# Kernel optimization log

Hardware: AMD Instinct MI355X
Metric: run time of the kernel (lower is better)

Reference implementation:

```python
import jax, jax.numpy as jnp
import numpy as np

B, S, D, H, HD, F = 2, 2048, 2048, 16, 128, 8192
EPS = 1e-5
THETA = 10000.0
NEG = -1e30


def _rmsnorm(x, w):
    v = jnp.mean(jnp.square(x.astype(jnp.float32)), axis=-1, keepdims=True)
    return (x.astype(jnp.float32) * jax.lax.rsqrt(v + EPS)).astype(x.dtype) * w


def _rope(x):
    # x: [B, S, H, HD]; llama-style rotate-half rotary embedding
    inv_freq = 1.0 / (THETA ** (jnp.arange(0, HD, 2, dtype=jnp.float32) / HD))
    ang = jnp.arange(S, dtype=jnp.float32)[:, None] * inv_freq[None, :]  # [S, HD//2]
    cos = jnp.concatenate([jnp.cos(ang), jnp.cos(ang)], axis=-1)[None, :, None, :]
    sin = jnp.concatenate([jnp.sin(ang), jnp.sin(ang)], axis=-1)[None, :, None, :]
    x1, x2 = jnp.split(x, 2, axis=-1)
    return x * cos + jnp.concatenate([-x2, x1], axis=-1) * sin


def _mlp(x, wg, wu, wd):
    # SiLU-gated HiggsAudioMLP: down(silu(gate(x)) * up(x))
    return (jax.nn.silu(x @ wg) * (x @ wu)) @ wd


def setup_inputs() -> dict:
    key = jax.random.key(0)
    ks = jax.random.split(key, 12)
    std = 0.02
    p = lambda k, shape: jax.random.normal(k, shape, dtype=jnp.float32) * std
    return {
        "hidden_states": jax.random.normal(ks[0], (B, S, D), dtype=jnp.float32),
        "audio_out_mask": jax.random.randint(ks[1], (B, S), 0, 2).astype(bool),
        "wq": p(ks[2], (D, H * HD)),
        "wk": p(ks[3], (D, H * HD)),
        "wv": p(ks[4], (D, H * HD)),
        "wo": p(ks[5], (H * HD, D)),
        "input_ln_w": jnp.ones((D,), jnp.float32),
        "post_ln_w": jnp.ones((D,), jnp.float32),
        "audio_post_ln_w": jnp.ones((D,), jnp.float32),
        "w_gate_t": p(ks[6], (D, F)),
        "w_up_t": p(ks[7], (D, F)),
        "w_down_t": p(ks[8], (F, D)),
        "w_gate_a": p(ks[9], (D, F)),
        "w_up_a": p(ks[10], (D, F)),
        "w_down_a": p(ks[11], (F, D)),
    }


def reference(hidden_states, audio_out_mask, wq, wk, wv, wo, input_ln_w, post_ln_w,
              audio_post_ln_w, w_gate_t, w_up_t, w_down_t, w_gate_a, w_up_a, w_down_a):
    # ---- self-attention block ----
    residual = hidden_states
    h = _rmsnorm(hidden_states, input_ln_w)
    q = _rope((h @ wq).reshape(B, S, H, HD))
    k = _rope((h @ wk).reshape(B, S, H, HD))
    v = (h @ wv).reshape(B, S, H, HD)
    scores = jnp.einsum("bqhd,bkhd->bhqk", q, k) / float(np.sqrt(HD))
    causal = jnp.tril(jnp.ones((S, S), bool))
    scores = jnp.where(causal[None, None], scores, NEG)
    attn = jax.nn.softmax(scores, axis=-1)
    ctx = jnp.einsum("bhqk,bkhd->bqhd", attn, v).reshape(B, S, H * HD)
    hidden_states = residual + ctx @ wo
    # ---- dual FFN, per-token routed by audio_out_mask ----
    residual = hidden_states
    text_out = _mlp(_rmsnorm(hidden_states, post_ln_w), w_gate_t, w_up_t, w_down_t)
    audio_out = _mlp(_rmsnorm(hidden_states, audio_post_ln_w), w_gate_a, w_up_a, w_down_a)
    return residual + jnp.where(audio_out_mask[..., None], audio_out, text_out)
```

## Files before the change

kernel.cpp:

```cpp
#include <hip/hip_runtime.h>


#define BB 2
#define SS 2048
#define DD 2048
#define HH 16
#define HDD 128
#define FF 8192
#define TT (BB*SS)
#define RPAD 4608

typedef unsigned short ushort_t;
typedef __bf16 bf16x8 __attribute__((ext_vector_type(8)));
typedef float f32x4 __attribute__((ext_vector_type(4)));

#define DEV static __device__ __forceinline__

DEV float bf2f(ushort_t u) { __bf16 b; __builtin_memcpy(&b, &u, 2); return (float)b; }
DEV ushort_t f2bf(float f) { __bf16 b = (__bf16)f; ushort_t u; __builtin_memcpy(&u, &b, 2); return u; }

DEV void gl_lds16(const ushort_t* g, ushort_t* l) {
    __builtin_amdgcn_global_load_lds((const __attribute__((address_space(1))) void*)g,
                                     (__attribute__((address_space(3))) void*)l, 16, 0, 0);
}

#define BARRIER() do { asm volatile("" ::: "memory"); __builtin_amdgcn_s_barrier(); asm volatile("" ::: "memory"); } while (0)
#define LGKM0()   asm volatile("s_waitcnt lgkmcnt(0)" ::: "memory")

__global__ __launch_bounds__(256) void partition_k(const unsigned char* __restrict__ raw,
                                                   int* __restrict__ perm,
                                                   int* __restrict__ header) {
    __shared__ int flag;
    __shared__ int ct[256], ca[256], st[256], sa[256];
    __shared__ int Nt_s, Na_s;
    const int tid = threadIdx.x;
    if (tid == 0) flag = 0;
    __syncthreads();
    int any = 0;
    for (int i = tid; i < TT; i += 256)
        if ((i & 3) != 0 && raw[i] != 0) any = 1;
    if (any) atomicOr(&flag, 1);
    __syncthreads();
    const int is_byte = flag;
    auto mget = [&](int r) -> int {
        return is_byte ? (raw[r] != 0) : (((const int*)raw)[r] != 0);
    };
    int c0 = 0, c1 = 0;
#pragma unroll
    for (int i = 0; i < 16; ++i) {
        if (mget(tid * 16 + i)) c1++; else c0++;
    }
    ct[tid] = c0; ca[tid] = c1;
    __syncthreads();
    if (tid == 0) {
        int at = 0, aa = 0;
        for (int i = 0; i < 256; ++i) {
            st[i] = at; at += ct[i];
            sa[i] = aa; aa += ca[i];
        }
        Nt_s = at; Na_s = aa;
    }
    __syncthreads();
    const int Nt = Nt_s, Na = Na_s;
    const int A0 = (Nt + 255) & ~255;
    const int live = A0 + ((Na + 255) & ~255);
    int pt = st[tid], pa = A0 + sa[tid];
#pragma unroll
    for (int i = 0; i < 16; ++i) {
        const int r = tid * 16 + i;
        if (mget(r)) perm[pa++] = r; else perm[pt++] = r;
    }
    for (int i = Nt + tid; i < A0; i += 256) perm[i] = -1;
    for (int i = A0 + Na + tid; i < RPAD; i += 256) perm[i] = -1;
    if (tid == 0) { header[0] = Nt; header[1] = A0; header[2] = Na; header[3] = live; }
}

struct ConvSeg { const float* in; ushort_t* out; int K, N, cumEnd; };
struct ConvArgs { ConvSeg s[10]; };

__global__ __launch_bounds__(256) void convw_all(ConvArgs a) {
    __shared__ float t[32][33];
    int bid = blockIdx.x;
    int i = 0;
    while (bid >= a.s[i].cumEnd) ++i;
    const int base = (i == 0) ? 0 : a.s[i - 1].cumEnd;
    const int local = bid - base;
    const float* __restrict__ in = a.s[i].in;
    ushort_t* __restrict__ out = a.s[i].out;
    const int K = a.s[i].K, N = a.s[i].N;
    const int ntile = N >> 5;
    const int n0 = (local % ntile) * 32, k0 = (local / ntile) * 32;
    const int tx = threadIdx.x & 31, ty = threadIdx.x >> 5;
#pragma unroll
    for (int j = 0; j < 4; ++j)
        t[ty + 8 * j][tx] = in[(size_t)(k0 + ty + 8 * j) * N + n0 + tx];
    __syncthreads();
#pragma unroll
    for (int j = 0; j < 4; ++j)
        out[(size_t)(n0 + ty + 8 * j) * K + k0 + tx] = f2bf(t[tx][ty + 8 * j]);
}

__global__ __launch_bounds__(256) void rmsnorm_k(const float* __restrict__ x,
                                                 const float* __restrict__ wt,
                                                 ushort_t* __restrict__ out) {
    const int row = blockIdx.x, tid = threadIdx.x;
    const float4* xr = (const float4*)(x + (size_t)row * DD);
    float4 v0 = xr[tid * 2], v1 = xr[tid * 2 + 1];
    float ss = v0.x * v0.x + v0.y * v0.y + v0.z * v0.z + v0.w * v0.w
             + v1.x * v1.x + v1.y * v1.y + v1.z * v1.z + v1.w * v1.w;
#pragma unroll
    for (int d = 1; d < 64; d <<= 1) ss += __shfl_xor(ss, d);
    __shared__ float red[4];
    if ((tid & 63) == 0) red[tid >> 6] = ss;
    __syncthreads();
    const float tot = red[0] + red[1] + red[2] + red[3];
    const float sc = rsqrtf(tot * (1.0f / DD) + 1e-5f);
    const float4* wr = (const float4*)wt;
    float4 w0 = wr[tid * 2], w1 = wr[tid * 2 + 1];
    ushort_t* o = out + (size_t)row * DD + tid * 8;
    o[0] = f2bf(v0.x * sc * w0.x); o[1] = f2bf(v0.y * sc * w0.y);
    o[2] = f2bf(v0.z * sc * w0.z); o[3] = f2bf(v0.w * sc * w0.w);
    o[4] = f2bf(v1.x * sc * w1.x); o[5] = f2bf(v1.y * sc * w1.y);
    o[6] = f2bf(v1.z * sc * w1.z); o[7] = f2bf(v1.w * sc * w1.w);
}

__global__ __launch_bounds__(256) void rmsnorm_gather(const float* __restrict__ x,
                                                      const float* __restrict__ wt_text,
                                                      const float* __restrict__ wt_audio,
                                                      const int* __restrict__ perm,
                                                      const int* __restrict__ header,
                                                      ushort_t* __restrict__ out) {
    const int i = blockIdx.x, tid = threadIdx.x;
    const int p = perm[i];
    ushort_t* o = out + (size_t)i * DD + tid * 8;
    if (p < 0) {
#pragma unroll
        for (int j = 0; j < 8; ++j) o[j] = 0;
        return;
    }
    const float* wt = (i < header[1]) ? wt_text : wt_audio;
    const float4* xr = (const float4*)(x + (size_t)p * DD);
    float4 v0 = xr[tid * 2], v1 = xr[tid * 2 + 1];
    float ss = v0.x * v0.x + v0.y * v0.y + v0.z * v0.z + v0.w * v0.w
             + v1.x * v1.x + v1.y * v1.y + v1.z * v1.z + v1.w * v1.w;
#pragma unroll
    for (int d = 1; d < 64; d <<= 1) ss += __shfl_xor(ss, d);
    __shared__ float red[4];
    if ((tid & 63) == 0) red[tid >> 6] = ss;
    __syncthreads();
    const float tot = red[0] + red[1] + red[2] + red[3];
    const float sc = rsqrtf(tot * (1.0f / DD) + 1e-5f);
    const float4* wr = (const float4*)wt;
    float4 w0 = wr[tid * 2], w1 = wr[tid * 2 + 1];
    o[0] = f2bf(v0.x * sc * w0.x); o[1] = f2bf(v0.y * sc * w0.y);
    o[2] = f2bf(v0.z * sc * w0.z); o[3] = f2bf(v0.w * sc * w0.w);
    o[4] = f2bf(v1.x * sc * w1.x); o[5] = f2bf(v1.y * sc * w1.y);
    o[6] = f2bf(v1.z * sc * w1.z); o[7] = f2bf(v1.w * sc * w1.w);
}

__global__ __launch_bounds__(256) void rope_tab(float* __restrict__ cosb,
                                                float* __restrict__ sinb) {
    const int idx = blockIdx.x * 256 + threadIdx.x;
    const int s = idx >> 6, i = idx & 63;
    const float inv = powf(10000.0f, -(float)i * (1.0f / 64.0f));
    const float ang = (float)s * inv;
    cosb[idx] = cosf(ang);
    sinb[idx] = sinf(ang);
}

__global__ __launch_bounds__(256) void rope_qk(ushort_t* __restrict__ qb,
                                               ushort_t* __restrict__ kb,
                                               const float* __restrict__ cosb,
                                               const float* __restrict__ sinb) {
    const int gid = blockIdx.x * 256 + threadIdx.x;
    ushort_t* x = (gid < TT * 1024) ? qb : kb;
    const int g = gid & (TT * 1024 - 1);
    const int row = g >> 10, p = g & 1023;
    const int h = p >> 6, d = p & 63;
    const int s = row & (SS - 1);
    const size_t base = (size_t)row * DD + h * HDD + d;
    const float x1 = bf2f(x[base]), x2 = bf2f(x[base + 64]);
    const float c = cosb[s * 64 + d], sn = sinb[s * 64 + d];
    x[base]      = f2bf(x1 * c - x2 * sn);
    x[base + 64] = f2bf(x2 * c + x1 * sn);
}

template <int EPI>
__global__ __launch_bounds__(512, 2) void gemm_nt8(
    const ushort_t* __restrict__ A, const ushort_t* __restrict__ W,
    int K, ushort_t* __restrict__ o0, ushort_t* __restrict__ o1,
    ushort_t* __restrict__ o2, float* __restrict__ Cf,
    const float* __restrict__ resid) {
    const int nwg = gridDim.x * gridDim.y;
    int bid = blockIdx.y * gridDim.x + blockIdx.x;
    bid = (bid & 7) * (nwg >> 3) + (bid >> 3);
    const int bxx = bid % gridDim.x;
    const int byy = bid / gridDim.x;
    const int m0 = byy * 256;
    int kind = 0, n0;
    const ushort_t* B;
    if (EPI == 0) {
        kind = bxx >> 4;
        n0 = (bxx & 15) * 128;
        B = W + (size_t)kind * DD * DD + (size_t)n0 * K;
    } else {
        n0 = bxx * 128;
        B = W + (size_t)n0 * K;
    }
    __shared__ ushort_t smem[49152];
    const int tid = threadIdx.x;
    const int w = tid >> 6, lane = tid & 63;
    const int wm = w >> 2, wn = w & 3;
    const int f16 = lane & 15, g4 = lane >> 4;
    const int rl = tid >> 3;
    const int cc8 = (((tid & 7) ^ ((tid >> 3) & 7)) * 8);
    const ushort_t* gA = A + (size_t)m0 * K;

    auto stageAq = [&](int buf, int k0, int q) {
        gl_lds16(gA + (size_t)(q * 64 + rl) * K + k0 + cc8,
                 &smem[buf * 24576 + q * 4096 + w * 512]);
    };
    auto stageB2 = [&](int buf, int k0) {
#pragma unroll
        for (int j = 0; j < 2; ++j)
            gl_lds16(B + (size_t)(j * 64 + rl) * K + k0 + cc8,
                     &smem[buf * 24576 + 16384 + j * 4096 + w * 512]);
    };

    const int aBase = (wm * 128 + f16) * 64;
    const int bBase = (wn * 32 + f16) * 64;
    int cswz[2];
    cswz[0] = ((g4 ^ (f16 & 7)) * 8);
    cswz[1] = (((4 + g4) ^ (f16 & 7)) * 8);

    f32x4 acc[8][2] = {};
    bf16x8 af[4][2], bfr[2][2];

    stageAq(0, 0, 0); stageAq(0, 0, 1); stageAq(0, 0, 2); stageAq(0, 0, 3);
    stageB2(0, 0);
    stageAq(1, 64, 0); stageAq(1, 64, 2); stageB2(1, 64);
    asm volatile("s_waitcnt vmcnt(4)" ::: "memory");
    BARRIER();

    const int nt = K / 64;
    for (int t = 0; t < nt; ++t) {
        const int cur = t & 1;
        const int ab = cur * 24576, bb = cur * 24576 + 16384;
#pragma unroll
        for (int m = 0; m < 4; ++m)
#pragma unroll
            for (int ks = 0; ks < 2; ++ks)
                af[m][ks] = *(const bf16x8*)&smem[ab + aBase + m * 1024 + cswz[ks]];
#pragma unroll
        for (int np = 0; np < 2; ++np)
#pragma unroll
            for (int ks = 0; ks < 2; ++ks)
                bfr[np][ks] = *(const bf16x8*)&smem[bb + bBase + np * 1024 + cswz[ks]];
        if (t + 1 < nt) {
            stageAq(1 - cur, (t + 1) * 64, 1);
            stageAq(1 - cur, (t + 1) * 64, 3);
        }
        BARRIER();
        LGKM0();
        __builtin_amdgcn_s_setprio(1);
#pragma unroll
        for (int m = 0; m < 4; ++m)
#pragma unroll
            for (int np = 0; np < 2; ++np)
#pragma unroll
                for (int ks = 0; ks < 2; ++ks)
                    acc[m][np] = __builtin_amdgcn_mfma_f32_16x16x32_bf16(af[m][ks], bfr[np][ks], acc[m][np], 0, 0, 0);
        __builtin_amdgcn_s_setprio(0);
        BARRIER();
#pragma unroll
        for (int m = 0; m < 4; ++m)
#pragma unroll
            for (int ks = 0; ks < 2; ++ks)
                af[m][ks] = *(const bf16x8*)&smem[ab + aBase + (4 + m) * 1024 + cswz[ks]];
        if (t + 2 < nt) {
            stageAq(cur, (t + 2) * 64, 0);
            stageAq(cur, (t + 2) * 64, 2);
            stageB2(cur, (t + 2) * 64);
        }
        BARRIER();
        LGKM0();
        __builtin_amdgcn_s_setprio(1);
#pragma unroll
        for (int m = 0; m < 4; ++m)
#pragma unroll
            for (int np = 0; np < 2; ++np)
#pragma unroll
                for (int ks = 0; ks < 2; ++ks)
                    acc[4 + m][np] = __builtin_amdgcn_mfma_f32_16x16x32_bf16(af[m][ks], bfr[np][ks], acc[4 + m][np], 0, 0, 0);
        __builtin_amdgcn_s_setprio(0);
        if (t + 2 < nt) { asm volatile("s_waitcnt vmcnt(4)" ::: "memory"); }
        else            { asm volatile("s_waitcnt vmcnt(0)" ::: "memory"); }
        BARRIER();
    }

#pragma unroll
    for (int m = 0; m < 8; ++m)
#pragma unroll
        for (int np = 0; np < 2; ++np)
#pragma unroll
            for (int j = 0; j < 4; ++j) {
                const int r = m0 + wm * 128 + m * 16 + g4 * 4 + j;
                const int c = n0 + wn * 32 + np * 16 + f16;
                const float v = acc[m][np][j];
                if (EPI == 0) {
                    const ushort_t vb = f2bf(v);
                    if (kind == 0)      o0[(size_t)r * DD + c] = vb;
                    else if (kind == 1) o1[(size_t)r * DD + c] = vb;
                    else {
                        const int b = r >> 11, s = r & (SS - 1), h = c >> 7, d = c & 127;
                        o2[(((size_t)(b * HH + h) * HDD + d) << 11) + s] = vb;
                    }
                } else {
                    const size_t idx = (size_t)r * DD + c;
                    Cf[idx] = resid[idx] + v;
                }
            }
}

__global__ __launch_bounds__(256, 2) void gemm_down_c(
    const ushort_t* __restrict__ A, const ushort_t* __restrict__ Bt_text,
    const ushort_t* __restrict__ Bt_audio, float* __restrict__ C,
    const int* __restrict__ perm, const int* __restrict__ header) {
    const int m0 = blockIdx.y * 128;
    if (m0 >= header[3]) return;
    const ushort_t* Bt = (m0 >= header[1]) ? Bt_audio : Bt_text;
    __shared__ ushort_t As[128 * 32];
    __shared__ ushort_t Bs[128 * 32];
    const int tid = threadIdx.x;
    const int w = tid >> 6, lane = tid & 63;
    const int n0 = blockIdx.x * 128;
    const int wr = w >> 1, wc = w & 1;
    f32x4 acc[4][4] = {};
    const ushort_t* gA = A + (size_t)m0 * FF;
    const ushort_t* gB = Bt + (size_t)n0 * FF;
    const int c0 = tid, c1 = 256 + tid;
    const int r0 = c0 >> 2, o0 = (c0 & 3) * 8;
    const int r1 = c1 >> 2, o1 = (c1 & 3) * 8;
    ushort_t* lA0 = &As[(w * 64) * 8];
    ushort_t* lA1 = &As[(256 + w * 64) * 8];
    ushort_t* lB0 = &Bs[(w * 64) * 8];
    ushort_t* lB1 = &Bs[(256 + w * 64) * 8];
    for (int k0 = 0; k0 < FF; k0 += 32) {
        __syncthreads();
        gl_lds16(gA + (size_t)r0 * FF + k0 + o0, lA0);
        gl_lds16(gA + (size_t)r1 * FF + k0 + o1, lA1);
        gl_lds16(gB + (size_t)r0 * FF + k0 + o0, lB0);
        gl_lds16(gB + (size_t)r1 * FF + k0 + o1, lB1);
        asm volatile("s_waitcnt vmcnt(0)" ::: "memory");
        __syncthreads();
        const int ko = (lane >> 4) * 8;
        const int ra = wr * 64 + (lane & 15);
        const int rb = wc * 64 + (lane & 15);
        bf16x8 af[4], bfv[4];
#pragma unroll
        for (int mi = 0; mi < 4; ++mi) af[mi] = *(const bf16x8*)&As[(ra + mi * 16) * 32 + ko];
#pragma unroll
        for (int ni = 0; ni < 4; ++ni) bfv[ni] = *(const bf16x8*)&Bs[(rb + ni * 16) * 32 + ko];
#pragma unroll
        for (int mi = 0; mi < 4; ++mi)
#pragma unroll
            for (int ni = 0; ni < 4; ++ni)
                acc[mi][ni] = __builtin_amdgcn_mfma_f32_16x16x32_bf16(af[mi], bfv[ni], acc[mi][ni], 0, 0, 0);
    }
    const int cl = lane & 15, r4 = (lane >> 4) * 4;
#pragma unroll
    for (int mi = 0; mi < 4; ++mi)
#pragma unroll
        for (int ni = 0; ni < 4; ++ni)
#pragma unroll
            for (int j = 0; j < 4; ++j) {
                const int r = m0 + wr * 64 + mi * 16 + r4 + j;
                const int p = perm[r];
                if (p >= 0) {
                    const int c = n0 + wc * 64 + ni * 16 + cl;
                    float* q = C + (size_t)p * DD + c;
                    *q = *q + acc[mi][ni][j];
                }
            }
}

__global__ __launch_bounds__(512, 2) void gemm_gu8(
    const ushort_t* __restrict__ A,
    const ushort_t* __restrict__ Bg_t, const ushort_t* __restrict__ Bu_t,
    const ushort_t* __restrict__ Bg_a, const ushort_t* __restrict__ Bu_a,
    ushort_t* __restrict__ act, const int* __restrict__ header) {
    const int nwg = gridDim.x * gridDim.y;
    int bid = blockIdx.y * gridDim.x + blockIdx.x;
    bid = (bid & 7) * (nwg >> 3) + (bid >> 3);
    const int bx = bid % 64;
    const int by = bid / 64;
    const int m0 = by * 256;
    if (m0 >= header[3]) return;
    const bool audio = (m0 >= header[1]);
    const ushort_t* Bg = audio ? Bg_a : Bg_t;
    const ushort_t* Bu = audio ? Bu_a : Bu_t;
    const int n0g = bx * 128;

    __shared__ ushort_t smem[65536];
    const int tid = threadIdx.x;
    const int w = tid >> 6, lane = tid & 63;
    const int wm = w >> 2, wn = w & 3;
    const int f16 = lane & 15, g4 = lane >> 4;

    const int rl = tid >> 3;
    const int cc8 = (((tid & 7) ^ ((tid >> 3) & 7)) * 8);
    const int wchunk = w * 64;

    const ushort_t* gA = A + (size_t)m0 * DD;

    auto stageA_h = [&](int buf, int k0, int h) {
#pragma unroll
        for (int j = 0; j < 2; ++j) {
            const int r = h * 128 + j * 64 + rl;
            gl_lds16(gA + (size_t)r * DD + k0 + cc8,
                     &smem[buf * 32768 + h * 8192 + (j * 512 + wchunk) * 8]);
        }
    };
    auto stageB_h = [&](int buf, int k0, int h) {
#pragma unroll
        for (int j = 0; j < 2; ++j) {
            const int br = h * 128 + j * 64 + rl;
            const int ty = (br >> 4) & 1;
            const int grow = ((br >> 5) << 4) + (br & 15);
            const ushort_t* src = (ty ? Bu : Bg) + (size_t)(n0g + grow) * DD + k0 + cc8;
            gl_lds16(src, &smem[buf * 32768 + 16384 + h * 8192 + (j * 512 + wchunk) * 8]);
        }
    };

    const int aBase = (wm * 128 + f16) * 64;
    const int bBase = (wn * 64 + f16) * 64;
    int cswz[2];
    cswz[0] = ((g4 ^ (f16 & 7)) * 8);
    cswz[1] = (((4 + g4) ^ (f16 & 7)) * 8);

    f32x4 acc[8][4] = {};
    bf16x8 af[4][2], b0[2][2], b1[2][2];

    stageA_h(0, 0, 0); stageA_h(0, 0, 1);
    stageB_h(0, 0, 0); stageB_h(0, 0, 1);
    stageA_h(1, 64, 0); stageB_h(1, 64, 0);
    asm volatile("s_waitcnt vmcnt(4)" ::: "memory");
    BARRIER();

    const int nt = DD / 64;
    for (int t = 0; t < nt; ++t) {
        const int buf = t & 1, obuf = buf ^ 1;
        const int ab = buf * 32768, bb = buf * 32768 + 16384;
        const int k1 = (t + 1) * 64, k2 = (t + 2) * 64;
        const bool pf1 = (t + 1) < nt, pf2 = (t + 2) < nt;
#pragma unroll
        for (int m = 0; m < 4; ++m)
#pragma unroll
            for (int ks = 0; ks < 2; ++ks)
                af[m][ks] = *(const bf16x8*)&smem[ab + aBase + m * 1024 + cswz[ks]];
#pragma unroll
        for (int n = 0; n < 2; ++n)
#pragma unroll
            for (int ks = 0; ks < 2; ++ks)
                b0[n][ks] = *(const bf16x8*)&smem[bb + bBase + n * 1024 + cswz[ks]];
        if (pf1) stageA_h(obuf, k1, 1);
        BARRIER();
        LGKM0();
        __builtin_amdgcn_s_setprio(1);
#pragma unroll
        for (int m = 0; m < 4; ++m)
#pragma unroll
            for (int n = 0; n < 2; ++n)
#pragma unroll
                for (int ks = 0; ks < 2; ++ks)
                    acc[m][n] = __builtin_amdgcn_mfma_f32_16x16x32_bf16(af[m][ks], b0[n][ks], acc[m][n], 0, 0, 0);
        __builtin_amdgcn_s_setprio(0);
        BARRIER();
#pragma unroll
        for (int n = 0; n < 2; ++n)
#pragma unroll
            for (int ks = 0; ks < 2; ++ks)
                b1[n][ks] = *(const bf16x8*)&smem[bb + bBase + (2 + n) * 1024 + cswz[ks]];
        if (pf1) stageB_h(obuf, k1, 1);
        BARRIER();
        LGKM0();
        __builtin_amdgcn_s_setprio(1);
#pragma unroll
        for (int m = 0; m < 4; ++m)
#pragma unroll
            for (int n = 0; n < 2; ++n)
#pragma unroll
                for (int ks = 0; ks < 2; ++ks)
                    acc[m][2 + n] = __builtin_amdgcn_mfma_f32_16x16x32_bf16(af[m][ks], b1[n][ks], acc[m][2 + n], 0, 0, 0);
        __builtin_amdgcn_s_setprio(0);
        BARRIER();
#pragma unroll
        for (int m = 0; m < 4; ++m)
#pragma unroll
            for (int ks = 0; ks < 2; ++ks)
                af[m][ks] = *(const bf16x8*)&smem[ab + aBase + (4 + m) * 1024 + cswz[ks]];
        BARRIER();
        LGKM0();
        __builtin_amdgcn_s_setprio(1);
#pragma unroll
        for (int m = 0; m < 4; ++m)
#pragma unroll
            for (int n = 0; n < 2; ++n)
#pragma unroll
                for (int ks = 0; ks < 2; ++ks)
                    acc[4 + m][n] = __builtin_amdgcn_mfma_f32_16x16x32_bf16(af[m][ks], b0[n][ks], acc[4 + m][n], 0, 0, 0);
        __builtin_amdgcn_s_setprio(0);
        BARRIER();
        if (pf2) { stageA_h(buf, k2, 0); stageB_h(buf, k2, 0); }
        BARRIER();
        __builtin_amdgcn_s_setprio(1);
#pragma unroll
        for (int m = 0; m < 4; ++m)
#pragma unroll
            for (int n = 0; n < 2; ++n)
#pragma unroll
                for (int ks = 0; ks < 2; ++ks)
                    acc[4 + m][2 + n] = __builtin_amdgcn_mfma_f32_16x16x32_bf16(af[m][ks], b1[n][ks], acc[4 + m][2 + n], 0, 0, 0);
        __builtin_amdgcn_s_setprio(0);
        if (pf2)      { asm volatile("s_waitcnt vmcnt(4)" ::: "memory"); }
        else if (pf1) { asm volatile("s_waitcnt vmcnt(0)" ::: "memory"); }
        BARRIER();
    }

    const int r4 = g4 * 4;
#pragma unroll
    for (int m = 0; m < 8; ++m)
#pragma unroll
        for (int np = 0; np < 2; ++np) {
            const int f = n0g + (wn * 2 + np) * 16 + f16;
#pragma unroll
            for (int j = 0; j < 4; ++j) {
                const int r = m0 + wm * 128 + m * 16 + r4 + j;
                const float g = acc[m][np * 2][j], u = acc[m][np * 2 + 1][j];
                act[(size_t)r * FF + f] = f2bf(g / (1.0f + __expf(-g)) * u);
            }
        }
}

__global__ __launch_bounds__(512, 2) void attn_k(
    const ushort_t* __restrict__ qb, const ushort_t* __restrict__ kb,
    const ushort_t* __restrict__ vt, ushort_t* __restrict__ ctx) {
    __shared__ ushort_t Ks[2][64 * 128];
    __shared__ ushort_t Vs[2][128 * 64];
    __shared__ ushort_t Pw[8][16 * 64];
    const int tid = threadIdx.x, w = tid >> 6, lane = tid & 63;
    const int qt = gridDim.x - 1 - blockIdx.x;
    const int bh = blockIdx.y, b = bh >> 4, h = bh & 15;
    const int q0 = qt * 128 + w * 16;
    const int f16 = lane & 15, g4 = lane >> 4;
    bf16x8 aq[4];
    {
        const ushort_t* qr = qb + ((size_t)(b * SS + q0 + f16)) * DD + h * HDD + g4 * 8;
#pragma unroll
        for (int ko = 0; ko < 4; ++ko) aq[ko] = *(const bf16x8*)(qr + ko * 32);
    }
    auto stageKV = [&](int bufi, int kt) {
        const int sk0 = kt * 64;
#pragma unroll
        for (int i = 0; i < 2; ++i) {
            const int c = i * 512 + tid;
            const int csrc = ((c & 15) ^ ((c >> 4) & 7)) * 8;
            gl_lds16(kb + ((size_t)(b * SS + sk0 + (c >> 4))) * DD + h * HDD + csrc,
                     &Ks[bufi][(i * 512 + w * 64) * 8]);
        }
#pragma unroll
        for (int i = 0; i < 2; ++i) {
            const int c = i * 512 + tid;
            const int csrc = ((c & 7) ^ ((c >> 3) & 7)) * 8;
            gl_lds16(vt + ((size_t)((b * HH + h) * HDD + (c >> 3))) * SS + sk0 + csrc,
                     &Vs[bufi][(i * 512 + w * 64) * 8]);
        }
    };
    f32x4 o[8] = {};
    float mrow[4] = {-3e38f, -3e38f, -3e38f, -3e38f};
    float lrow[4] = {};
    const int nkv = 2 * qt + 2;
    stageKV(0, 0);
    for (int kt = 0; kt < nkv; ++kt) {
        const int cur = kt & 1;
        if (kt < nkv - 1) {
            stageKV(cur ^ 1, kt + 1);
            asm volatile("s_waitcnt vmcnt(4)" ::: "memory");
        } else {
            asm volatile("s_waitcnt vmcnt(0)" ::: "memory");
        }
        BARRIER();
        f32x4 s[4] = {};
#pragma unroll
        for (int ko = 0; ko < 4; ++ko)
#pragma unroll
            for (int ni = 0; ni < 4; ++ni) {
                bf16x8 bk = *(const bf16x8*)&Ks[cur][(ni * 16 + f16) * 128 + (((ko * 4 + g4) ^ (f16 & 7)) * 8)];
                s[ni] = __builtin_amdgcn_mfma_f32_16x16x32_bf16(aq[ko], bk, s[ni], 0, 0, 0);
            }
        const float scale = 0.08838834764831843f;
#pragma unroll
        for (int ni = 0; ni < 4; ++ni)
#pragma unroll
            for (int j = 0; j < 4; ++j) {
                float v = s[ni][j] * scale;
                const int kg = kt * 64 + ni * 16 + f16;
                const int qg = q0 + g4 * 4 + j;
                if (kg > qg) v = -1e30f;
                s[ni][j] = v;
            }
#pragma unroll
        for (int j = 0; j < 4; ++j) {
            float tm = fmaxf(fmaxf(s[0][j], s[1][j]), fmaxf(s[2][j], s[3][j]));
#pragma unroll
            for (int dd = 1; dd < 16; dd <<= 1) tm = fmaxf(tm, __shfl_xor(tm, dd));
            if (!__all(tm <= mrow[j] + 8.0f)) {
                const float mn = fmaxf(mrow[j], tm);
                const float corr = __expf(mrow[j] - mn);
                lrow[j] *= corr;
#pragma unroll
                for (int di = 0; di < 8; ++di) o[di][j] *= corr;
                mrow[j] = mn;
            }
            float sum = 0.f;
#pragma unroll
            for (int ni = 0; ni < 4; ++ni) {
                const float p = __expf(s[ni][j] - mrow[j]);
                s[ni][j] = p;
                sum += p;
            }
#pragma unroll
            for (int dd = 1; dd < 16; dd <<= 1) sum += __shfl_xor(sum, dd);
            lrow[j] += sum;
        }
#pragma unroll
        for (int ni = 0; ni < 4; ++ni)
#pragma unroll
            for (int j = 0; j < 4; ++j) {
                const int prow = g4 * 4 + j;
                const int pcb = ni * 2 + (f16 >> 3);
                Pw[w][prow * 64 + ((pcb ^ (prow & 7)) * 8) + (f16 & 7)] = f2bf(s[ni][j]);
            }
#pragma unroll
        for (int ks = 0; ks < 2; ++ks) {
            bf16x8 pa = *(const bf16x8*)&Pw[w][f16 * 64 + (((ks * 4 + g4) ^ (f16 & 7)) * 8)];
#pragma unroll
            for (int di = 0; di < 8; ++di) {
                bf16x8 bv = *(const bf16x8*)&Vs[cur][(di * 16 + f16) * 64 + (((ks * 4 + g4) ^ (f16 & 7)) * 8)];
                o[di] = __builtin_amdgcn_mfma_f32_16x16x32_bf16(pa, bv, o[di], 0, 0, 0);
            }
        }
        BARRIER();
    }
    float inv[4];
#pragma unroll
    for (int j = 0; j < 4; ++j) inv[j] = 1.0f / lrow[j];
#pragma unroll
    for (int di = 0; di < 8; ++di)
#pragma unroll
        for (int j = 0; j < 4; ++j) {
            const int r = q0 + g4 * 4 + j;
            ctx[((size_t)(b * SS + r)) * DD + h * HDD + di * 16 + f16] = f2bf(o[di][j] * inv[j]);
        }
}

extern "C" void kernel_launch(void* const* d_in, const int* in_sizes, int n_in,
                              void* d_out, int out_size, void* d_ws, size_t ws_size,
                              hipStream_t stream) {
    (void)in_sizes; (void)n_in; (void)out_size; (void)ws_size;
    const float* hs  = (const float*)d_in[0];
    const unsigned char* mask_raw = (const unsigned char*)d_in[1];
    const float* wq  = (const float*)d_in[2];
    const float* wk  = (const float*)d_in[3];
    const float* wv  = (const float*)d_in[4];
    const float* wo  = (const float*)d_in[5];
    const float* iln = (const float*)d_in[6];
    const float* pln = (const float*)d_in[7];
    const float* aln = (const float*)d_in[8];
    const float* wgt = (const float*)d_in[9];
    const float* wut = (const float*)d_in[10];
    const float* wdt = (const float*)d_in[11];
    const float* wga = (const float*)d_in[12];
    const float* wua = (const float*)d_in[13];
    const float* wda = (const float*)d_in[14];

    const size_t SZ_W1 = (size_t)DD * DD * 2;
    const size_t SZ_W2 = (size_t)DD * FF * 2;
    const size_t SZ_A  = (size_t)TT * DD * 2;

    char* ws = (char*)d_ws;
    size_t off = 0;
    auto take = [&](size_t n) { char* p = ws + off; off += n; return p; };
    ushort_t* wq_t  = (ushort_t*)take(SZ_W1);
    ushort_t* wk_t  = (ushort_t*)take(SZ_W1);
    ushort_t* wv_t  = (ushort_t*)take(SZ_W1);
    ushort_t* wo_t  = (ushort_t*)take(SZ_W1);
    ushort_t* wg_tb = (ushort_t*)take(SZ_W2);
    ushort_t* wu_tb = (ushort_t*)take(SZ_W2);
    ushort_t* wd_tb = (ushort_t*)take(SZ_W2);
    ushort_t* wg_ab = (ushort_t*)take(SZ_W2);
    ushort_t* wu_ab = (ushort_t*)take(SZ_W2);
    ushort_t* wd_ab = (ushort_t*)take(SZ_W2);
    char* actreg = take(6 * SZ_A);
    float* cosb = (float*)take((size_t)SS * 64 * 4);
    float* sinb = (float*)take((size_t)SS * 64 * 4);
    int* perm   = (int*)take(RPAD * 4);
    int* header = (int*)take(64);

    ushort_t* h_bf = (ushort_t*)(actreg);
    ushort_t* qb   = (ushort_t*)(actreg + 1 * SZ_A);
    ushort_t* kb   = (ushort_t*)(actreg + 2 * SZ_A);
    ushort_t* vt   = (ushort_t*)(actreg + 3 * SZ_A);
    ushort_t* ctx  = (ushort_t*)(actreg + 4 * SZ_A);
    ushort_t* hn_c  = (ushort_t*)(actreg);
    ushort_t* act_c = (ushort_t*)(actreg + (size_t)RPAD * DD * 2);

    const dim3 blk(256);

    partition_k<<<1, blk, 0, stream>>>(mask_raw, perm, header);

    ConvArgs ca;
    int cum = 0;
    auto seg = [&](int i, const float* in, ushort_t* out, int K, int N) {
        cum += (N / 32) * (K / 32);
        ca.s[i] = ConvSeg{in, out, K, N, cum};
    };
    seg(0, wq, wq_t, DD, DD);
    seg(1, wk, wk_t, DD, DD);
    seg(2, wv, wv_t, DD, DD);
    seg(3, wo, wo_t, DD, DD);
    seg(4, wgt, wg_tb, DD, FF);
    seg(5, wut, wu_tb, DD, FF);
    seg(6, wdt, wd_tb, FF, DD);
    seg(7, wga, wg_ab, DD, FF);
    seg(8, wua, wu_ab, DD, FF);
    seg(9, wda, wd_ab, FF, DD);
    convw_all<<<cum, blk, 0, stream>>>(ca);

    rope_tab<<<(SS * 64) / 256, blk, 0, stream>>>(cosb, sinb);

    rmsnorm_k<<<TT, blk, 0, stream>>>(hs, iln, h_bf);
    gemm_nt8<0><<<dim3(48, TT / 256), dim3(512), 0, stream>>>(
        h_bf, wq_t, DD, qb, kb, vt, nullptr, nullptr);
    rope_qk<<<(2 * TT * 1024) / 256, blk, 0, stream>>>(qb, kb, cosb, sinb);
    attn_k<<<dim3(SS / 128, BB * HH), dim3(512), 0, stream>>>(qb, kb, vt, ctx);
    gemm_nt8<1><<<dim3(DD / 128, TT / 256), dim3(512), 0, stream>>>(
        ctx, wo_t, DD, nullptr, nullptr, nullptr, (float*)d_out, hs);

    rmsnorm_gather<<<RPAD, blk, 0, stream>>>((const float*)d_out, pln, aln, perm, header, hn_c);
    gemm_gu8<<<dim3(FF / 128, RPAD / 256), dim3(512), 0, stream>>>(hn_c, wg_tb, wu_tb, wg_ab, wu_ab, act_c, header);
    gemm_down_c<<<dim3(DD / 128, RPAD / 128), blk, 0, stream>>>(act_c, wd_tb, wd_ab, (float*)d_out, perm, header);
}
```

Measured before the change: 1.103 ms.

## Fuse weight conversion, rope table and input rmsnorm into one prep kernel; reorder B prefetch

Merges three preprocessing kernels (weight transpose/convert, rope cos/sin table, input RMSNorm) into a single launch that selects work by block index. This removes two kernel launches and the idle gaps between them. Separately, in one GEMM's main loop the B-tile prefetch for stage k2 now issues one phase earlier than the A-tile prefetch, to spread global loads across the pipeline. The earlier B staging needs the target buffer to be free by then, which risks a race if the schedule assumptions do not hold.

```diff
diff --git a/kernel.cpp b/kernel.cpp
--- a/kernel.cpp
+++ b/kernel.cpp
@@ -78,50 +78,61 @@
 struct ConvSeg { const float* in; ushort_t* out; int K, N, cumEnd; };
 struct ConvArgs { ConvSeg s[10]; };
 
-__global__ __launch_bounds__(256) void convw_all(ConvArgs a) {
+__global__ __launch_bounds__(256) void prep_all(ConvArgs a, int convEnd,
+                                                float* __restrict__ cosb,
+                                                float* __restrict__ sinb,
+                                                const float* __restrict__ hs,
+                                                const float* __restrict__ iln,
+                                                ushort_t* __restrict__ h_bf) {
     __shared__ float t[32][33];
-    int bid = blockIdx.x;
-    int i = 0;
-    while (bid >= a.s[i].cumEnd) ++i;
-    const int base = (i == 0) ? 0 : a.s[i - 1].cumEnd;
-    const int local = bid - base;
-    const float* __restrict__ in = a.s[i].in;
-    ushort_t* __restrict__ out = a.s[i].out;
-    const int K = a.s[i].K, N = a.s[i].N;
-    const int ntile = N >> 5;
-    const int n0 = (local % ntile) * 32, k0 = (local / ntile) * 32;
-    const int tx = threadIdx.x & 31, ty = threadIdx.x >> 5;
-#pragma unroll
-    for (int j = 0; j < 4; ++j)
-        t[ty + 8 * j][tx] = in[(size_t)(k0 + ty + 8 * j) * N + n0 + tx];
-    __syncthreads();
-#pragma unroll
-    for (int j = 0; j < 4; ++j)
-        out[(size_t)(n0 + ty + 8 * j) * K + k0 + tx] = f2bf(t[tx][ty + 8 * j]);
-}
-
-__global__ __launch_bounds__(256) void rmsnorm_k(const float* __restrict__ x,
-                                                 const float* __restrict__ wt,
-                                                 ushort_t* __restrict__ out) {
-    const int row = blockIdx.x, tid = threadIdx.x;
-    const float4* xr = (const float4*)(x + (size_t)row * DD);
-    float4 v0 = xr[tid * 2], v1 = xr[tid * 2 + 1];
-    float ss = v0.x * v0.x + v0.y * v0.y + v0.z * v0.z + v0.w * v0.w
-             + v1.x * v1.x + v1.y * v1.y + v1.z * v1.z + v1.w * v1.w;
-#pragma unroll
-    for (int d = 1; d < 64; d <<= 1) ss += __shfl_xor(ss, d);
-    __shared__ float red[4];
-    if ((tid & 63) == 0) red[tid >> 6] = ss;
-    __syncthreads();
-    const float tot = red[0] + red[1] + red[2] + red[3];
-    const float sc = rsqrtf(tot * (1.0f / DD) + 1e-5f);
-    const float4* wr = (const float4*)wt;
-    float4 w0 = wr[tid * 2], w1 = wr[tid * 2 + 1];
-    ushort_t* o = out + (size_t)row * DD + tid * 8;
-    o[0] = f2bf(v0.x * sc * w0.x); o[1] = f2bf(v0.y * sc * w0.y);
-    o[2] = f2bf(v0.z * sc * w0.z); o[3] = f2bf(v0.w * sc * w0.w);
-    o[4] = f2bf(v1.x * sc * w1.x); o[5] = f2bf(v1.y * sc * w1.y);
-    o[6] = f2bf(v1.z * sc * w1.z); o[7] = f2bf(v1.w * sc * w1.w);
+    const int bid = blockIdx.x;
+    const int tid = threadIdx.x;
+    if (bid < convEnd) {
+        int i = 0;
+        while (bid >= a.s[i].cumEnd) ++i;
+        const int base = (i == 0) ? 0 : a.s[i - 1].cumEnd;
+        const int local = bid - base;
+        const float* __restrict__ in = a.s[i].in;
+        ushort_t* __restrict__ out = a.s[i].out;
+        const int K = a.s[i].K, N = a.s[i].N;
+        const int ntile = N >> 5;
+        const int n0 = (local % ntile) * 32, k0 = (local / ntile) * 32;
+        const int tx = tid & 31, ty = tid >> 5;
+#pragma unroll
+        for (int j = 0; j < 4; ++j)
+            t[ty + 8 * j][tx] = in[(size_t)(k0 + ty + 8 * j) * N + n0 + tx];
+        __syncthreads();
+#pragma unroll
+        for (int j = 0; j < 4; ++j)
+            out[(size_t)(n0 + ty + 8 * j) * K + k0 + tx] = f2bf(t[tx][ty + 8 * j]);
+    } else if (bid < convEnd + 512) {
+        const int idx = (bid - convEnd) * 256 + tid;
+        const int s = idx >> 6, i = idx & 63;
+        const float inv = powf(10000.0f, -(float)i * (1.0f / 64.0f));
+        const float ang = (float)s * inv;
+        cosb[idx] = cosf(ang);
+        sinb[idx] = sinf(ang);
+    } else {
+        const int row = bid - convEnd - 512;
+        const float4* xr = (const float4*)(hs + (size_t)row * DD);
+        float4 v0 = xr[tid * 2], v1 = xr[tid * 2 + 1];
+        float ss = v0.x * v0.x + v0.y * v0.y + v0.z * v0.z + v0.w * v0.w
+                 + v1.x * v1.x + v1.y * v1.y + v1.z * v1.z + v1.w * v1.w;
+#pragma unroll
+        for (int d = 1; d < 64; d <<= 1) ss += __shfl_xor(ss, d);
+        float* red = &t[0][0];
+        if ((tid & 63) == 0) red[tid >> 6] = ss;
+        __syncthreads();
+        const float tot = red[0] + red[1] + red[2] + red[3];
+        const float sc = rsqrtf(tot * (1.0f / DD) + 1e-5f);
+        const float4* wr = (const float4*)iln;
+        float4 w0 = wr[tid * 2], w1 = wr[tid * 2 + 1];
+        ushort_t* o = h_bf + (size_t)row * DD + tid * 8;
+        o[0] = f2bf(v0.x * sc * w0.x); o[1] = f2bf(v0.y * sc * w0.y);
+        o[2] = f2bf(v0.z * sc * w0.z); o[3] = f2bf(v0.w * sc * w0.w);
+        o[4] = f2bf(v1.x * sc * w1.x); o[5] = f2bf(v1.y * sc * w1.y);
+        o[6] = f2bf(v1.z * sc * w1.z); o[7] = f2bf(v1.w * sc * w1.w);
+    }
 }
 
 __global__ __launch_bounds__(256) void rmsnorm_gather(const float* __restrict__ x,
@@ -156,16 +167,6 @@
     o[2] = f2bf(v0.z * sc * w0.z); o[3] = f2bf(v0.w * sc * w0.w);
     o[4] = f2bf(v1.x * sc * w1.x); o[5] = f2bf(v1.y * sc * w1.y);
     o[6] = f2bf(v1.z * sc * w1.z); o[7] = f2bf(v1.w * sc * w1.w);
-}
-
-__global__ __launch_bounds__(256) void rope_tab(float* __restrict__ cosb,
-                                                float* __restrict__ sinb) {
-    const int idx = blockIdx.x * 256 + threadIdx.x;
-    const int s = idx >> 6, i = idx & 63;
-    const float inv = powf(10000.0f, -(float)i * (1.0f / 64.0f));
-    const float ang = (float)s * inv;
-    cosb[idx] = cosf(ang);
-    sinb[idx] = sinf(ang);
 }
 
 __global__ __launch_bounds__(256) void rope_qk(ushort_t* __restrict__ qb,
@@ -499,6 +500,7 @@
 #pragma unroll
             for (int ks = 0; ks < 2; ++ks)
                 af[m][ks] = *(const bf16x8*)&smem[ab + aBase + (4 + m) * 1024 + cswz[ks]];
+        if (pf2) stageB_h(buf, k2, 0);
         BARRIER();
         LGKM0();
         __builtin_amdgcn_s_setprio(1);
@@ -511,7 +513,7 @@
                     acc[4 + m][n] = __builtin_amdgcn_mfma_f32_16x16x32_bf16(af[m][ks], b0[n][ks], acc[4 + m][n], 0, 0, 0);
         __builtin_amdgcn_s_setprio(0);
         BARRIER();
-        if (pf2) { stageA_h(buf, k2, 0); stageB_h(buf, k2, 0); }
+        if (pf2) stageA_h(buf, k2, 0);
         BARRIER();
         __builtin_amdgcn_s_setprio(1);
 #pragma unroll
@@ -735,11 +737,8 @@
     seg(7, wga, wg_ab, DD, FF);
     seg(8, wua, wu_ab, DD, FF);
     seg(9, wda, wd_ab, FF, DD);
-    convw_all<<<cum, blk, 0, stream>>>(ca);
-
-    rope_tab<<<(SS * 64) / 256, blk, 0, stream>>>(cosb, sinb);
-
-    rmsnorm_k<<<TT, blk, 0, stream>>>(hs, iln, h_bf);
+    prep_all<<<cum + 512 + TT, blk, 0, stream>>>(ca, cum, cosb, sinb, hs, iln, h_bf);
+
     gemm_nt8<0><<<dim3(48, TT / 256), dim3(512), 0, stream>>>(
         h_bf, wq_t, DD, qb, kb, vt, nullptr, nullptr);
     rope_qk<<<(2 * TT * 1024) / 256, blk, 0, stream>>>(qb, kb, cosb, sinb);
```

Result: no change. 1.096 ms (-0.6%).
